# Kernel tuning notes

Hardware: AMD Instinct MI355X
Metric: run time of the kernel (lower is better)

## Reference

```python
import jax, jax.numpy as jnp
import numpy as np
jax.config.update("jax_enable_x64", True)

B, T, EPROJS, ODIM, U = 16, 1600, 512, 2048, 200
RISK_FACTOR = 0.1
NEG = float('-inf')


def _safe_lse0(x):
    # logsumexp over axis 0, safe for all -inf columns (no NaN in fwd or bwd)
    m = jnp.max(x, axis=0)
    ms = jnp.where(jnp.isinf(m), 0.0, m)
    s = jnp.sum(jnp.exp(x - ms), axis=0)
    out = ms + jnp.log(jnp.where(s == 0, 1.0, s))
    return jnp.where(s == 0, NEG, out)


def _log_sub_exp(a, b):
    # faithful port of log_substraction_exp: log(exp(a) - exp(b))
    mask1 = (~jnp.isinf(a)) & (~jnp.isinf(b))
    a_ = jnp.where(mask1, a, -1.0)
    b_ = jnp.where(mask1, b, -2.0)
    tmp = b_ + jnp.log(jnp.exp(a_ - b_) - 1.0)
    a_ = jnp.where(jnp.isinf(tmp), -2000.0, a_)
    b_ = jnp.where(jnp.isinf(tmp), -2001.0, b_)
    ans1 = b_ + jnp.log(jnp.exp(a_ - b_) - 1.0)
    ans = jnp.where(mask1, ans1, NEG)
    ans = jnp.where((~jnp.isinf(a)) & jnp.isinf(b), a, ans)
    return ans


def _ctc_bayes_loss(hs_pad, W, bvec, hlens, ys_pad):
    Bn, Tn, _ = hs_pad.shape
    Un = ys_pad.shape[1]
    S = 2 * Un + 1  # extended CTC state count (blank-interleaved)
    logits = hs_pad @ W.T + bvec
    logprob = jax.nn.log_softmax(logits, axis=-1).astype(jnp.float64)  # [B,T,V]
    ysc = jnp.where(ys_pad < 0, 0, ys_pad)
    olens = jnp.sum(ys_pad >= 0, axis=1)
    lp_blank = logprob[:, :, 0]                                        # [B,T]
    lp_label = jnp.take_along_axis(logprob, ysc[:, None, :], axis=2)   # [B,T,U]
    # emission log-probs on extended states: even=blank, odd=label u=(s-1)//2
    pair = jnp.stack([jnp.broadcast_to(lp_blank[:, :, None], (Bn, Tn, Un)), lp_label], axis=-1).reshape(Bn, Tn, 2 * Un)
    em = jnp.concatenate([pair, lp_blank[:, :, None]], axis=-1)        # [B,T,S]
    # skip transition (s-2 -> s) allowed into odd s with differing neighbor label
    allow_odd = jnp.concatenate([jnp.zeros((Bn, 1), bool), ysc[:, 1:] != ysc[:, :-1]], axis=1)
    allow = jnp.concatenate([jnp.stack([jnp.zeros((Bn, Un), bool), allow_odd], -1).reshape(Bn, 2 * Un), jnp.zeros((Bn, 1), bool)], axis=1)
    allow_fwd = jnp.concatenate([allow[:, 2:], jnp.zeros((Bn, 2), bool)], axis=1)
    em_t = jnp.transpose(em, (1, 0, 2))                                # [T,B,S]
    ninf2 = jnp.full((Bn, S), NEG, jnp.float64)
    alpha0 = ninf2.at[:, 0].set(em_t[0, :, 0]).at[:, 1].set(em_t[0, :, 1])

    def alpha_step(carry, e):
        s1 = jnp.concatenate([jnp.full((Bn, 1), NEG, jnp.float64), carry[:, :-1]], 1)
        s2 = jnp.concatenate([jnp.full((Bn, 2), NEG, jnp.float64), carry[:, :-2]], 1)
        s2 = jnp.where(allow, s2, NEG)
        new = e + _safe_lse0(jnp.stack([carry, s1, s2], 0))
        return new, new

    _, alpha_rest = jax.lax.scan(alpha_step, alpha0, em_t[1:])
    alpha_all = jnp.concatenate([alpha0[None], alpha_rest], 0)         # [T,B,S]

    sidx = jnp.arange(S)[None, :]
    fin = jnp.where((sidx == 2 * olens[:, None]) | (sidx == 2 * olens[:, None] - 1), 0.0, NEG)
    em_nxt = jnp.concatenate([em_t[1:], em_t[-1:]], 0)                 # em_nxt[t] = em_t[t+1]
    ts = jnp.arange(Tn - 1, -1, -1)

    def beta_step(carry, x):
        t, e_next = x
        g = e_next + carry
        g1 = jnp.concatenate([g[:, 1:], jnp.full((Bn, 1), NEG, jnp.float64)], 1)
        g2 = jnp.concatenate([g[:, 2:], jnp.full((Bn, 2), NEG, jnp.float64)], 1)
        g2 = jnp.where(allow_fwd, g2, NEG)
        new = _safe_lse0(jnp.stack([g, g1, g2], 0))
        new = jnp.where((t == hlens - 1)[:, None], fin, new)
        return new, new

    _, beta_rev = jax.lax.scan(beta_step, ninf2, (ts, em_nxt[::-1]))
    beta_all = beta_rev[::-1]                                          # [T,B,S]

    alpha_u = jnp.transpose(alpha_all, (1, 2, 0))[:, 1::2, :]          # [B,U,T]
    beta_u = jnp.transpose(beta_all, (1, 2, 0))[:, 1::2, :]
    valid = (jnp.arange(Un)[None, :, None] < olens[:, None, None]) & (jnp.arange(Tn)[None, None, :] < hlens[:, None, None])
    alpha_u = jnp.where(valid, alpha_u, NEG)
    beta_u = jnp.where(valid, beta_u, NEG)
    p = jnp.where(valid, jnp.transpose(lp_label, (0, 2, 1)), NEG)      # [B,U,T]
    beta_prime = jnp.concatenate([_log_sub_exp(beta_u[:, :, :-1], beta_u[:, :, 1:] + p[:, :, 1:]), beta_u[:, :, -1:]], axis=-1)
    risk = jnp.arange(1, Tn + 1, dtype=jnp.float64)[None, None, :] / hlens[:, None, None].astype(jnp.float64) * RISK_FACTOR
    loss_state = alpha_u + beta_prime + risk
    loss_state = jnp.where(jnp.isnan(loss_state), NEG, loss_state)
    # aggregate == 'time': logsumexp over t, pick last valid label position
    m = jnp.max(loss_state, axis=2)
    ms = jnp.where(jnp.isinf(m), 0.0, m)
    ssum = jnp.sum(jnp.exp(loss_state - ms[:, :, None]), axis=2)
    loss_u = jnp.where(ssum == 0, NEG, ms + jnp.log(jnp.where(ssum == 0, 1.0, ssum)))
    mask = jnp.isinf(loss_u)
    last = jnp.sum(~mask, axis=1) - 1
    loss_fsas = loss_u[jnp.arange(Bn), last]
    loss_fsas = jnp.where(hlens < olens, 0.0, loss_fsas)
    return jnp.mean(-loss_fsas)


def setup_inputs() -> dict:
    key = jax.random.key(0)
    k1, k2, k3, k4, k5, k6 = jax.random.split(key, 6)
    hs_pad = jax.random.normal(k1, (B, T, EPROJS), jnp.float32)
    W = jax.random.normal(k2, (ODIM, EPROJS), jnp.float32) * 0.05
    b = jnp.zeros((ODIM,), jnp.float32)
    hlens = (T - jax.random.randint(k3, (B,), 0, 200)).astype(jnp.int64)
    ys = jax.random.randint(k4, (B, U), 1, ODIM)
    olens = U - jax.random.randint(k5, (B,), 0, 20)
    ys_pad = jnp.where(jnp.arange(U)[None, :] < olens[:, None], ys, -1).astype(jnp.int64)
    ali = jax.random.randint(k6, (B, U), 0, T).astype(jnp.int64)
    return {"hs_pad": hs_pad, "W": W, "b": b, "hlens": hlens, "ys_pad": ys_pad, "ali": ali}


def reference(hs_pad, W, b, hlens, ys_pad, ali):
    # ali is unused for risk_strategy='time' (matches the torch module)
    return _ctc_bayes_loss(hs_pad, W, b, hlens, ys_pad)
```

## Files before the change

### kernel.cpp

```cpp
#include <hip/hip_runtime.h>
#include <math.h>


#define Bn    16
#define Tn    1600
#define NE    512
#define OD    2048
#define Un    200
#define Sn    401
#define NLAB  201
#define NGC   256

#define NEGINF (-INFINITY)
#define LSE_SUB_CONST_F (-2000.4586715f)

typedef short bf8_t  __attribute__((ext_vector_type(8)));
typedef float f32x4  __attribute__((ext_vector_type(4)));

__device__ __forceinline__ unsigned short f2bf(float x) {
    unsigned int u = __float_as_uint(x);
    unsigned int r = (u + 0x7FFFu + ((u >> 16) & 1u)) >> 16;
    return (unsigned short)r;
}
__device__ __forceinline__ void lse_merge_v(float& M, float& S, float v) {
    if (v > M) { S = S * __expf(M - v) + 1.f; M = v; }
    else       { S += __expf(v - M); }
}
__device__ __forceinline__ void lse_merge_ms(float& M, float& S, float m2, float s2) {
    if (s2 > 0.f) {
        if (m2 > M) { S = S * __expf(M - m2) + s2; M = m2; }
        else        { S += s2 * __expf(m2 - M); }
    }
}

__global__ __launch_bounds__(256)
void cast_hs_kernel(const float* __restrict__ src, unsigned short* __restrict__ dst, int n8) {
    int i = blockIdx.x * 256 + threadIdx.x;
    if (i >= n8) return;
    const float4* s4 = (const float4*)(src + (size_t)i * 8);
    float4 a = s4[0], b = s4[1];
    uint4 o;
    o.x = f2bf(a.x) | ((unsigned)f2bf(a.y) << 16);
    o.y = f2bf(a.z) | ((unsigned)f2bf(a.w) << 16);
    o.z = f2bf(b.x) | ((unsigned)f2bf(b.y) << 16);
    o.w = f2bf(b.z) | ((unsigned)f2bf(b.w) << 16);
    *(uint4*)(dst + (size_t)i * 8) = o;
}

__global__ __launch_bounds__(64)
void gather_kernel(const float* __restrict__ W, const float* __restrict__ bias,
                   const int* __restrict__ ys, unsigned short* __restrict__ Wgb,
                   float* __restrict__ biasg)
{
    const int b = blockIdx.x, j = blockIdx.y, tid = threadIdx.x;
    int col = -1;
    if (j == 0) col = 0;
    else if (j <= Un) { int y = ys[b * Un + j - 1]; col = (y < 0) ? 0 : y; }
    unsigned short* dst = Wgb + ((size_t)b * NGC + j) * NE;
    if (col >= 0) {
        const float* srcc = W + (size_t)col * NE;
        #pragma unroll
        for (int it = 0; it < 8; ++it) dst[tid + it * 64] = f2bf(srcc[tid + it * 64]);
    } else {
        #pragma unroll
        for (int it = 0; it < 8; ++it) dst[tid + it * 64] = 0;
    }
    if (tid == 0) biasg[b * NGC + j] = (col >= 0) ? bias[col] : 0.f;
}

#define KCH  64
#define ASTR 72

__global__ __launch_bounds__(256, 2)
void gemm_main_kernel(const unsigned short* __restrict__ hsb,
                      const unsigned short* __restrict__ Wb,
                      const float* __restrict__ bias,
                      float* __restrict__ Pm, float* __restrict__ Ps)
{
    __shared__ union {
        struct { unsigned short A[128 * ASTR]; unsigned short B[128 * ASTR]; } t;
        struct { float m[128 * 33]; float s[128 * 33]; } r;
    } sh;
    const int tid  = threadIdx.x;
    const int lane = tid & 63, w = tid >> 6;
    const int mw = w & 1, nw = w >> 1;
    const int quad = lane >> 4, lc = lane & 15;
    const int row0 = blockIdx.x * 128;
    const int c0   = blockIdx.y * 128;

    f32x4 acc[4][4];
    #pragma unroll
    for (int mi = 0; mi < 4; ++mi)
        #pragma unroll
        for (int ni = 0; ni < 4; ++ni) acc[mi][ni] = (f32x4)0.f;

    for (int kc = 0; kc < NE / KCH; ++kc) {
        __syncthreads();
        #pragma unroll
        for (int i = 0; i < 4; ++i) {
            int idx = tid + i * 256;
            int r = idx >> 3, c8 = idx & 7;
            *(uint4*)&sh.t.A[r * ASTR + c8 * 8] =
                *(const uint4*)&hsb[(size_t)(row0 + r) * NE + kc * KCH + c8 * 8];
            *(uint4*)&sh.t.B[r * ASTR + c8 * 8] =
                *(const uint4*)&Wb[(size_t)(c0 + r) * NE + kc * KCH + c8 * 8];
        }
        __syncthreads();
        #pragma unroll
        for (int ks = 0; ks < 2; ++ks) {
            bf8_t af[4], bg[4];
            #pragma unroll
            for (int mi = 0; mi < 4; ++mi)
                af[mi] = *(const bf8_t*)&sh.t.A[(mw * 64 + mi * 16 + lc) * ASTR + ks * 32 + quad * 8];
            #pragma unroll
            for (int ni = 0; ni < 4; ++ni)
                bg[ni] = *(const bf8_t*)&sh.t.B[(nw * 64 + ni * 16 + lc) * ASTR + ks * 32 + quad * 8];
            #pragma unroll
            for (int mi = 0; mi < 4; ++mi)
                #pragma unroll
                for (int ni = 0; ni < 4; ++ni)
                    acc[mi][ni] = __builtin_amdgcn_mfma_f32_16x16x32_bf16(af[mi], bg[ni], acc[mi][ni], 0, 0, 0);
        }
    }
    __syncthreads();
    float bcol[4];
    #pragma unroll
    for (int ni = 0; ni < 4; ++ni) bcol[ni] = bias[c0 + nw * 64 + ni * 16 + lc];
    #pragma unroll
    for (int mi = 0; mi < 4; ++mi)
        #pragma unroll
        for (int r = 0; r < 4; ++r) {
            float M = NEGINF, S = 0.f;
            #pragma unroll
            for (int ni = 0; ni < 4; ++ni) lse_merge_v(M, S, acc[mi][ni][r] + bcol[ni]);
            int rl = mw * 64 + mi * 16 + quad * 4 + r;
            sh.r.m[rl * 33 + nw * 16 + lc] = M;
            sh.r.s[rl * 33 + nw * 16 + lc] = S;
        }
    __syncthreads();
    if (tid < 128) {
        float M = NEGINF, S = 0.f;
        #pragma unroll 4
        for (int j = 0; j < 32; ++j) lse_merge_ms(M, S, sh.r.m[tid * 33 + j], sh.r.s[tid * 33 + j]);
        Pm[(size_t)blockIdx.y * 25600 + row0 + tid] = M;
        Ps[(size_t)blockIdx.y * 25600 + row0 + tid] = S;
    }
}

__global__ __launch_bounds__(256)
void lse_reduce_kernel(const float* __restrict__ Pm, const float* __restrict__ Ps,
                       float* __restrict__ lse)
{
    int row = blockIdx.x * 256 + threadIdx.x;
    float M = NEGINF, S = 0.f;
    #pragma unroll 4
    for (int nt = 0; nt < 16; ++nt)
        lse_merge_ms(M, S, Pm[(size_t)nt * 25600 + row], Ps[(size_t)nt * 25600 + row]);
    lse[row] = M + logf(S);
}

__global__ __launch_bounds__(256, 2)
void gemm_label_kernel(const unsigned short* __restrict__ hsb,
                       const unsigned short* __restrict__ Wgb,
                       const float* __restrict__ biasg, const float* __restrict__ lse,
                       float* __restrict__ lpl, float* __restrict__ lpbk)
{
    __shared__ unsigned short shA[64 * ASTR];
    __shared__ unsigned short shB[128 * ASTR];
    const int tid  = threadIdx.x;
    const int lane = tid & 63, w = tid >> 6;
    const int mw = w & 1, nw = w >> 1;
    const int quad = lane >> 4, lc = lane & 15;
    const int b  = blockIdx.x / 25, mt = blockIdx.x % 25;
    const int r0 = b * Tn + mt * 64;
    const int c0 = blockIdx.y * 128;

    f32x4 acc[2][4];
    #pragma unroll
    for (int mi = 0; mi < 2; ++mi)
        #pragma unroll
        for (int ni = 0; ni < 4; ++ni) acc[mi][ni] = (f32x4)0.f;

    const unsigned short* Wgbb = Wgb + (size_t)b * NGC * NE;
    for (int kc = 0; kc < NE / KCH; ++kc) {
        __syncthreads();
        #pragma unroll
        for (int i = 0; i < 2; ++i) {
            int idx = tid + i * 256;
            int r = idx >> 3, c8 = idx & 7;
            *(uint4*)&shA[r * ASTR + c8 * 8] =
                *(const uint4*)&hsb[(size_t)(r0 + r) * NE + kc * KCH + c8 * 8];
        }
        #pragma unroll
        for (int i = 0; i < 4; ++i) {
            int idx = tid + i * 256;
            int r = idx >> 3, c8 = idx & 7;
            *(uint4*)&shB[r * ASTR + c8 * 8] =
                *(const uint4*)&Wgbb[(size_t)(c0 + r) * NE + kc * KCH + c8 * 8];
        }
        __syncthreads();
        #pragma unroll
        for (int ks = 0; ks < 2; ++ks) {
            bf8_t af[2], bg[4];
            #pragma unroll
            for (int mi = 0; mi < 2; ++mi)
                af[mi] = *(const bf8_t*)&shA[(mw * 32 + mi * 16 + lc) * ASTR + ks * 32 + quad * 8];
            #pragma unroll
            for (int ni = 0; ni < 4; ++ni)
                bg[ni] = *(const bf8_t*)&shB[(nw * 64 + ni * 16 + lc) * ASTR + ks * 32 + quad * 8];
            #pragma unroll
            for (int mi = 0; mi < 2; ++mi)
                #pragma unroll
                for (int ni = 0; ni < 4; ++ni)
                    acc[mi][ni] = __builtin_amdgcn_mfma_f32_16x16x32_bf16(af[mi], bg[ni], acc[mi][ni], 0, 0, 0);
        }
    }
    #pragma unroll
    for (int mi = 0; mi < 2; ++mi)
        #pragma unroll
        for (int r = 0; r < 4; ++r) {
            int row = r0 + mw * 32 + mi * 16 + quad * 4 + r;
            float lsv = lse[row];
            #pragma unroll
            for (int ni = 0; ni < 4; ++ni) {
                int col = c0 + nw * 64 + ni * 16 + lc;
                if (col < NLAB) {
                    float v = acc[mi][ni][r] + biasg[b * NGC + col] - lsv;
                    if (col == 0) lpbk[row] = v;
                    else          lpl[(size_t)row * Un + (col - 1)] = v;
                }
            }
        }
}

#define IDX(s) ((s) + 2)

__device__ __forceinline__ float lse2f(float a, float b) {
    float mx = fmaxf(a, b);
    if (isinf(mx)) return NEGINF;
    return mx + __logf(__expf(a - mx) + __expf(b - mx));
}
__device__ __forceinline__ float lse3f(float v0, float v1, float v2) {
    float mx = fmaxf(v0, fmaxf(v1, v2));
    if (isinf(mx)) return NEGINF;
    return mx + __logf(__expf(v0 - mx) + __expf(v1 - mx) + __expf(v2 - mx));
}

#define STEP_BAR() do { \
    asm volatile("s_waitcnt lgkmcnt(0)" ::: "memory"); \
    __builtin_amdgcn_s_barrier(); \
    __builtin_amdgcn_sched_barrier(0); \
} while (0)

__global__ __launch_bounds__(256)
void scan_kernel(const float* __restrict__ lpl, const float* __restrict__ lpbk,
                 const int* __restrict__ hlens, const int* __restrict__ ys,
                 float* __restrict__ ast, float* __restrict__ bst)
{
    __shared__ float buf[2][408];
    __shared__ int   sh_olen, sh_hlen;

    const int b    = blockIdx.x & (Bn - 1);
    const int role = blockIdx.x >> 4;
    const int tid  = threadIdx.x;

    if (tid == 0) {
        int o = 0;
        for (int u = 0; u < Un; u++) if (ys[b * Un + u] >= 0) o++;
        sh_olen = o;
        sh_hlen = hlens[b];
    }
    for (int idx = tid; idx < 408; idx += 256) {
        buf[0][idx] = NEGINF;
        buf[1][idx] = NEGINF;
    }
    bool a1allow = false;
    if (tid >= 1 && tid < Un) {
        int y0 = ys[b * Un + tid - 1]; if (y0 < 0) y0 = 0;
        int y1 = ys[b * Un + tid];     if (y1 < 0) y1 = 0;
        a1allow = (y0 != y1);
    }
    bool a2allow = false;
    if (tid + 1 >= 1 && tid + 1 < Un) {
        int y0 = ys[b * Un + tid];     if (y0 < 0) y0 = 0;
        int y1 = ys[b * Un + tid + 1]; if (y1 < 0) y1 = 0;
        a2allow = (y0 != y1);
    }
    __syncthreads();

    const float* lplb = lpl + (size_t)b * Tn * Un;
    const float* lpbb = lpbk + (size_t)b * Tn;
    const int s0 = 2 * tid, s1 = 2 * tid + 1;
    const bool v0ok = (s0 < Sn);
    const bool v1ok = (s1 < Sn);
    const int  olen = sh_olen, hlen = sh_hlen;
    const int  ustar = olen - 1;

    if (role == 0) {
        float* as = ast + (size_t)b * Tn;
        if (tid == 0) { buf[0][IDX(0)] = lpbb[0]; buf[0][IDX(1)] = lplb[0]; }
        if (tid == ustar) as[0] = (tid == 0) ? lplb[0] : NEGINF;
        __syncthreads();

        #define ASTEP(T, EB, EO) do { \
            const float* cur = buf[((T) - 1) & 1]; \
            float* nxt = buf[(T) & 1]; \
            if (v0ok) { \
                float c1 = cur[IDX(s0) - 1]; \
                float c2 = cur[IDX(s0)], c3 = cur[IDX(s1)]; \
                float nv0 = lse2f(c2, c1); \
                if (!isinf(nv0)) nv0 += (EB); \
                nxt[IDX(s0)] = nv0; \
                if (v1ok) { \
                    float a1v2 = a1allow ? c1 : NEGINF; \
                    float nv1 = lse3f(c3, c2, a1v2); \
                    if (!isinf(nv1)) nv1 += (EO); \
                    nxt[IDX(s1)] = nv1; \
                    if (tid == ustar) as[T] = nv1; \
                } \
            } \
            STEP_BAR(); \
        } while (0)

        float ebA = lpbb[1], ebB = lpbb[2], ebC = lpbb[3], ebD = lpbb[4];
        float eoA = (tid < Un) ? lplb[(size_t)1 * Un + tid] : 0.f;
        float eoB = (tid < Un) ? lplb[(size_t)2 * Un + tid] : 0.f;
        float eoC = (tid < Un) ? lplb[(size_t)3 * Un + tid] : 0.f;
        float eoD = (tid < Un) ? lplb[(size_t)4 * Un + tid] : 0.f;
        int t = 1;
        for (; t + 3 < Tn; t += 4) {
            int rA = t + 4; if (rA > Tn - 1) rA = Tn - 1;
            float nbA = lpbb[rA];
            float noA = (tid < Un) ? lplb[(size_t)rA * Un + tid] : 0.f;
            ASTEP(t, ebA, eoA); ebA = nbA; eoA = noA;

            int rB = t + 5; if (rB > Tn - 1) rB = Tn - 1;
            float nbB = lpbb[rB];
            float noB = (tid < Un) ? lplb[(size_t)rB * Un + tid] : 0.f;
            ASTEP(t + 1, ebB, eoB); ebB = nbB; eoB = noB;

            int rC = t + 6; if (rC > Tn - 1) rC = Tn - 1;
            float nbC = lpbb[rC];
            float noC = (tid < Un) ? lplb[(size_t)rC * Un + tid] : 0.f;
            ASTEP(t + 2, ebC, eoC); ebC = nbC; eoC = noC;

            int rD = t + 7; if (rD > Tn - 1) rD = Tn - 1;
            float nbD = lpbb[rD];
            float noD = (tid < Un) ? lplb[(size_t)rD * Un + tid] : 0.f;
            ASTEP(t + 3, ebD, eoD); ebD = nbD; eoD = noD;
        }
        if (t < Tn)     ASTEP(t,     ebA, eoA);
        if (t + 1 < Tn) ASTEP(t + 1, ebB, eoB);
        if (t + 2 < Tn) ASTEP(t + 2, ebC, eoC);
        #undef ASTEP
    } else {
        float* bs = bst + (size_t)b * Tn;
        __syncthreads();

        #define BSTEP(T, EB, E0, E1) do { \
            const int it = (Tn - 1 - (T)) & 1; \
            const float* cur = buf[it]; \
            float* nxt = buf[it ^ 1]; \
            if (v0ok) { \
                float c0 = cur[IDX(s0)],     c1 = cur[IDX(s0) + 1]; \
                float c2 = cur[IDX(s0) + 2], c3 = cur[IDX(s0) + 3]; \
                float g0e = (EB) + c0; \
                float g1e = (E0) + c1; \
                float nv0 = lse2f(g0e, g1e); \
                float g0o = (E0) + c1; \
                float g1o = (EB) + c2; \
                float g2o = a2allow ? ((E1) + c3) : NEGINF; \
                float mh = fmaxf(g1o, g2o); \
                float h = NEGINF; \
                if (!isinf(mh)) \
                    h = mh + __logf(__expf(g1o - mh) + __expf(g2o - mh)); \
                float nv1 = v1ok ? lse3f(g0o, g1o, g2o) : NEGINF; \
                if ((T) == hlen - 1) { \
                    nv0 = (s0 == 2 * olen || s0 == 2 * olen - 1) ? 0.f : NEGINF; \
                    nv1 = (s1 == 2 * olen || s1 == 2 * olen - 1) ? 0.f : NEGINF; \
                } \
                nxt[IDX(s0)] = nv0; \
                if (v1ok) { \
                    nxt[IDX(s1)] = nv1; \
                    if (tid == ustar) { \
                        float bp; \
                        if ((T) >= hlen)          bp = NEGINF; \
                        else if ((T) == hlen - 1) bp = 0.f;  \
                        else if (isinf(g0o))      bp = h; \
                        else if (isinf(h))        bp = LSE_SUB_CONST_F; \
                        else { \
                            float sumlog = h - g0o; \
                            int k = (int)((__float_as_uint(fabsf(g0o)) >> 23) & 0xFF) - 127 - 53; \
                            if (k < -53) k = -53; \
                            bp = (sumlog > 709.7827f || sumlog < 0.69314718f * (float)k) \
                                 ? LSE_SUB_CONST_F : h; \
                        } \
                        bs[T] = bp; \
                    } \
                } \
            } \
            STEP_BAR(); \
        } while (0)

        float ebA = lpbb[Tn - 1];
        float e0A = (tid < Un)     ? lplb[(size_t)(Tn - 1) * Un + tid]     : 0.f;
        float e1A = (tid + 1 < Un) ? lplb[(size_t)(Tn - 1) * Un + tid + 1] : 0.f;
        float ebB = ebA, e0B = e0A, e1B = e1A;
        float ebC = lpbb[Tn - 2];
        float e0C = (tid < Un)     ? lplb[(size_t)(Tn - 2) * Un + tid]     : 0.f;
        float e1C = (tid + 1 < Un) ? lplb[(size_t)(Tn - 2) * Un + tid + 1] : 0.f;
        float ebD = lpbb[Tn - 3];
        float e0D = (tid < Un)     ? lplb[(size_t)(Tn - 3) * Un + tid]     : 0.f;
        float e1D = (tid + 1 < Un) ? lplb[(size_t)(Tn - 3) * Un + tid + 1] : 0.f;
        for (int t = Tn - 1; t > 0; t -= 4) {
            int rA = t - 3; if (rA < 0) rA = 0;
            float nbA = lpbb[rA];
            float n0A = (tid < Un)     ? lplb[(size_t)rA * Un + tid]     : 0.f;
            float n1A = (tid + 1 < Un) ? lplb[(size_t)rA * Un + tid + 1] : 0.f;
            BSTEP(t, ebA, e0A, e1A); ebA = nbA; e0A = n0A; e1A = n1A;

            int rB = t - 4; if (rB < 0) rB = 0;
            float nbB = lpbb[rB];
            float n0B = (tid < Un)     ? lplb[(size_t)rB * Un + tid]     : 0.f;
            float n1B = (tid + 1 < Un) ? lplb[(size_t)rB * Un + tid + 1] : 0.f;
            BSTEP(t - 1, ebB, e0B, e1B); ebB = nbB; e0B = n0B; e1B = n1B;

            int rC = t - 5; if (rC < 0) rC = 0;
            float nbC = lpbb[rC];
            float n0C = (tid < Un)     ? lplb[(size_t)rC * Un + tid]     : 0.f;
            float n1C = (tid + 1 < Un) ? lplb[(size_t)rC * Un + tid + 1] : 0.f;
            BSTEP(t - 2, ebC, e0C, e1C); ebC = nbC; e0C = n0C; e1C = n1C;

            int rD = t - 6; if (rD < 0) rD = 0;
            float nbD = lpbb[rD];
            float n0D = (tid < Un)     ? lplb[(size_t)rD * Un + tid]     : 0.f;
            float n1D = (tid + 1 < Un) ? lplb[(size_t)rD * Un + tid + 1] : 0.f;
            BSTEP(t - 3, ebD, e0D, e1D); ebD = nbD; e0D = n0D; e1D = n1D;
        }
        #undef BSTEP
    }
}

#define TCH 8
#define TPC (Tn / TCH)

__global__ __launch_bounds__(64)
void loss_kernel(const int* __restrict__ hlens, const int* __restrict__ ys,
                 const float* __restrict__ ast, const float* __restrict__ bst,
                 float* __restrict__ lossb)
{
    const int b = blockIdx.x, tid = threadIdx.x;
    __shared__ float sm[TCH], ss[TCH];
    __shared__ int sh_olen;
    if (tid == 0) {
        int o = 0;
        for (int u = 0; u < Un; u++) if (ys[b * Un + u] >= 0) o++;
        sh_olen = o;
    }
    __syncthreads();
    const int hlen = hlens[b];
    const float risk_c = 0.1f / (float)hlen;
    if (tid < TCH) {
        float m = NEGINF, s = 0.f;
        const float* as = ast + (size_t)b * Tn;
        const float* bs = bst + (size_t)b * Tn;
        const int t0 = tid * TPC, t1 = t0 + TPC;
        for (int t = t0; t < t1; ++t) {
            float v = as[t] + bs[t] + (float)(t + 1) * risk_c;
            if (!isinf(v)) lse_merge_v(m, s, v);
        }
        sm[tid] = m; ss[tid] = s;
    }
    __syncthreads();
    if (tid == 0) {
        float M = NEGINF, S = 0.f;
        #pragma unroll
        for (int c = 0; c < TCH; ++c) lse_merge_ms(M, S, sm[c], ss[c]);
        float lf = (S == 0.f) ? NEGINF : M + __logf(S);
        if (hlen < sh_olen) lf = 0.f;
        lossb[b] = lf;
    }
}

__global__ void finalize_kernel(const float* __restrict__ lossb, float* __restrict__ out) {
    if (threadIdx.x == 0 && blockIdx.x == 0) {
        float ssum = 0.f;
        for (int i = 0; i < Bn; i++) ssum += lossb[i];
        out[0] = -ssum / (float)Bn;
    }
}

extern "C" void kernel_launch(void* const* d_in, const int* in_sizes, int n_in,
                              void* d_out, int out_size, void* d_ws, size_t ws_size,
                              hipStream_t stream) {
    const float* hs    = (const float*)d_in[0];
    const float* W     = (const float*)d_in[1];
    const float* bias  = (const float*)d_in[2];
    const int*   hlens = (const int*)d_in[3];
    const int*   ys    = (const int*)d_in[4];
    float* out = (float*)d_out;

    char* p = (char*)d_ws;
    float* lpl    = (float*)p;  p += (size_t)25600 * Un * 4;
    float* lpbk   = (float*)p;  p += (size_t)25600 * 4;
    unsigned short* hsb = (unsigned short*)p; p += (size_t)25600 * NE * 2;
    unsigned short* Wb  = (unsigned short*)p; p += (size_t)OD * NE * 2;
    unsigned short* Wgb = (unsigned short*)p; p += (size_t)Bn * NGC * NE * 2;
    float* Pm    = (float*)p;   p += (size_t)16 * 25600 * 4;
    float* Ps    = (float*)p;   p += (size_t)16 * 25600 * 4;
    float* lse   = (float*)p;   p += (size_t)25600 * 4;
    float* biasg = (float*)p;   p += (size_t)Bn * NGC * 4;
    float* ast   = (float*)p;   p += (size_t)Bn * Tn * 4;
    float* bst   = (float*)p;   p += (size_t)Bn * Tn * 4;
    float* lossb = (float*)p;   p += 256;

    hipLaunchKernelGGL(cast_hs_kernel, dim3(6400), dim3(256), 0, stream,
                       hs, hsb, 25600 * NE / 8);
    hipLaunchKernelGGL(cast_hs_kernel, dim3(512), dim3(256), 0, stream,
                       W, Wb, OD * NE / 8);
    hipLaunchKernelGGL(gather_kernel, dim3(Bn, NGC), dim3(64), 0, stream,
                       W, bias, ys, Wgb, biasg);
    hipLaunchKernelGGL(gemm_main_kernel, dim3(200, 16), dim3(256), 0, stream,
                       hsb, Wb, bias, Pm, Ps);
    hipLaunchKernelGGL(lse_reduce_kernel, dim3(100), dim3(256), 0, stream,
                       Pm, Ps, lse);
    hipLaunchKernelGGL(gemm_label_kernel, dim3(400, 2), dim3(256), 0, stream,
                       hsb, Wgb, biasg, lse, lpl, lpbk);
    hipLaunchKernelGGL(scan_kernel, dim3(2 * Bn), dim3(256), 0, stream,
                       lpl, lpbk, hlens, ys, ast, bst);
    hipLaunchKernelGGL(loss_kernel, dim3(Bn), dim3(64), 0, stream,
                       hlens, ys, ast, bst, lossb);
    hipLaunchKernelGGL(finalize_kernel, dim3(1), dim3(64), 0, stream, lossb, out);
}
```

Baseline: 1.234 ms.

## Pad label logprobs to 256 stride, stage blank logprobs in LDS, shorten prefetch

Label log-probs are now stored with a padded row stride of 256, and the padding columns are zero-filled, so the scan kernels can load them without bounds checks. Blank log-probs for a batch are staged once into shared memory instead of being loaded from global memory every step. The scan's software prefetch depth drops from 4 to 2 steps, and the isinf guards before adding emissions are removed. This trims per-step instructions and global loads in the latency-bound serial scan, but prefetch latency hiding is shallower and the padded buffer is larger.

```diff
diff --git a/kernel.cpp b/kernel.cpp
--- a/kernel.cpp
+++ b/kernel.cpp
@@ -10,6 +10,7 @@
 #define Sn    401
 #define NLAB  201
 #define NGC   256
+#define LPS   256
 
 #define NEGINF (-INFINITY)
 #define LSE_SUB_CONST_F (-2000.4586715f)
@@ -224,11 +225,10 @@
             #pragma unroll
             for (int ni = 0; ni < 4; ++ni) {
                 int col = c0 + nw * 64 + ni * 16 + lc;
-                if (col < NLAB) {
-                    float v = acc[mi][ni][r] + biasg[b * NGC + col] - lsv;
-                    if (col == 0) lpbk[row] = v;
-                    else          lpl[(size_t)row * Un + (col - 1)] = v;
-                }
+                float v = acc[mi][ni][r] + biasg[b * NGC + col] - lsv;
+                if (col == 0)          lpbk[row] = v;
+                else if (col < NLAB)   lpl[(size_t)row * LPS + (col - 1)] = v;
+                else                   lpl[(size_t)row * LPS + (col - 1)] = 0.f;
             }
         }
 }
@@ -258,6 +258,7 @@
                  float* __restrict__ ast, float* __restrict__ bst)
 {
     __shared__ float buf[2][408];
+    __shared__ float ebs[Tn];
     __shared__ int   sh_olen, sh_hlen;
 
     const int b    = blockIdx.x & (Bn - 1);
@@ -274,6 +275,9 @@
         buf[0][idx] = NEGINF;
         buf[1][idx] = NEGINF;
     }
+    const float* lpbb = lpbk + (size_t)b * Tn;
+    for (int i = tid; i < Tn; i += 256) ebs[i] = lpbb[i];
+
     bool a1allow = false;
     if (tid >= 1 && tid < Un) {
         int y0 = ys[b * Un + tid - 1]; if (y0 < 0) y0 = 0;
@@ -288,8 +292,7 @@
     }
     __syncthreads();
 
-    const float* lplb = lpl + (size_t)b * Tn * Un;
-    const float* lpbb = lpbk + (size_t)b * Tn;
+    const float* lplb = lpl + (size_t)b * Tn * LPS;
     const int s0 = 2 * tid, s1 = 2 * tid + 1;
     const bool v0ok = (s0 < Sn);
     const bool v1ok = (s1 < Sn);
@@ -298,23 +301,21 @@
 
     if (role == 0) {
         float* as = ast + (size_t)b * Tn;
-        if (tid == 0) { buf[0][IDX(0)] = lpbb[0]; buf[0][IDX(1)] = lplb[0]; }
+        if (tid == 0) { buf[0][IDX(0)] = ebs[0]; buf[0][IDX(1)] = lplb[0]; }
         if (tid == ustar) as[0] = (tid == 0) ? lplb[0] : NEGINF;
         __syncthreads();
 
-        #define ASTEP(T, EB, EO) do { \
+        #define ASTEP(T, EO) do { \
             const float* cur = buf[((T) - 1) & 1]; \
             float* nxt = buf[(T) & 1]; \
             if (v0ok) { \
                 float c1 = cur[IDX(s0) - 1]; \
                 float c2 = cur[IDX(s0)], c3 = cur[IDX(s1)]; \
-                float nv0 = lse2f(c2, c1); \
-                if (!isinf(nv0)) nv0 += (EB); \
+                float nv0 = lse2f(c2, c1) + ebs[T]; \
                 nxt[IDX(s0)] = nv0; \
                 if (v1ok) { \
                     float a1v2 = a1allow ? c1 : NEGINF; \
-                    float nv1 = lse3f(c3, c2, a1v2); \
-                    if (!isinf(nv1)) nv1 += (EO); \
+                    float nv1 = lse3f(c3, c2, a1v2) + (EO); \
                     nxt[IDX(s1)] = nv1; \
                     if (tid == ustar) as[T] = nv1; \
                 } \
@@ -322,53 +323,35 @@
             STEP_BAR(); \
         } while (0)
 
-        float ebA = lpbb[1], ebB = lpbb[2], ebC = lpbb[3], ebD = lpbb[4];
-        float eoA = (tid < Un) ? lplb[(size_t)1 * Un + tid] : 0.f;
-        float eoB = (tid < Un) ? lplb[(size_t)2 * Un + tid] : 0.f;
-        float eoC = (tid < Un) ? lplb[(size_t)3 * Un + tid] : 0.f;
-        float eoD = (tid < Un) ? lplb[(size_t)4 * Un + tid] : 0.f;
-        int t = 1;
-        for (; t + 3 < Tn; t += 4) {
-            int rA = t + 4; if (rA > Tn - 1) rA = Tn - 1;
-            float nbA = lpbb[rA];
-            float noA = (tid < Un) ? lplb[(size_t)rA * Un + tid] : 0.f;
-            ASTEP(t, ebA, eoA); ebA = nbA; eoA = noA;
-
-            int rB = t + 5; if (rB > Tn - 1) rB = Tn - 1;
-            float nbB = lpbb[rB];
-            float noB = (tid < Un) ? lplb[(size_t)rB * Un + tid] : 0.f;
-            ASTEP(t + 1, ebB, eoB); ebB = nbB; eoB = noB;
-
-            int rC = t + 6; if (rC > Tn - 1) rC = Tn - 1;
-            float nbC = lpbb[rC];
-            float noC = (tid < Un) ? lplb[(size_t)rC * Un + tid] : 0.f;
-            ASTEP(t + 2, ebC, eoC); ebC = nbC; eoC = noC;
-
-            int rD = t + 7; if (rD > Tn - 1) rD = Tn - 1;
-            float nbD = lpbb[rD];
-            float noD = (tid < Un) ? lplb[(size_t)rD * Un + tid] : 0.f;
-            ASTEP(t + 3, ebD, eoD); ebD = nbD; eoD = noD;
-        }
-        if (t < Tn)     ASTEP(t,     ebA, eoA);
-        if (t + 1 < Tn) ASTEP(t + 1, ebB, eoB);
-        if (t + 2 < Tn) ASTEP(t + 2, ebC, eoC);
+        float eoA = lplb[(size_t)1 * LPS + tid];
+        float eoB = lplb[(size_t)2 * LPS + tid];
+        for (int t = 1; t < Tn; t += 2) {
+            int rA = t + 2; if (rA > Tn - 1) rA = Tn - 1;
+            float nA = lplb[(size_t)rA * LPS + tid];
+            ASTEP(t, eoA); eoA = nA;
+            if (t + 1 < Tn) {
+                int rB = t + 3; if (rB > Tn - 1) rB = Tn - 1;
+                float nB = lplb[(size_t)rB * LPS + tid];
+                ASTEP(t + 1, eoB); eoB = nB;
+            }
+        }
         #undef ASTEP
     } else {
         float* bs = bst + (size_t)b * Tn;
-        __syncthreads();
-
-        #define BSTEP(T, EB, E0, E1) do { \
+
+        #define BSTEP(T, E0, E1) do { \
             const int it = (Tn - 1 - (T)) & 1; \
             const float* cur = buf[it]; \
             float* nxt = buf[it ^ 1]; \
+            float eb = ebs[((T) + 1 > Tn - 1) ? (Tn - 1) : ((T) + 1)]; \
             if (v0ok) { \
                 float c0 = cur[IDX(s0)],     c1 = cur[IDX(s0) + 1]; \
                 float c2 = cur[IDX(s0) + 2], c3 = cur[IDX(s0) + 3]; \
-                float g0e = (EB) + c0; \
+                float g0e = eb + c0; \
                 float g1e = (E0) + c1; \
                 float nv0 = lse2f(g0e, g1e); \
                 float g0o = (E0) + c1; \
-                float g1o = (EB) + c2; \
+                float g1o = eb + c2; \
                 float g2o = a2allow ? ((E1) + c3) : NEGINF; \
                 float mh = fmaxf(g1o, g2o); \
                 float h = NEGINF; \
@@ -402,40 +385,21 @@
             STEP_BAR(); \
         } while (0)
 
-        float ebA = lpbb[Tn - 1];
-        float e0A = (tid < Un)     ? lplb[(size_t)(Tn - 1) * Un + tid]     : 0.f;
-        float e1A = (tid + 1 < Un) ? lplb[(size_t)(Tn - 1) * Un + tid + 1] : 0.f;
-        float ebB = ebA, e0B = e0A, e1B = e1A;
-        float ebC = lpbb[Tn - 2];
-        float e0C = (tid < Un)     ? lplb[(size_t)(Tn - 2) * Un + tid]     : 0.f;
-        float e1C = (tid + 1 < Un) ? lplb[(size_t)(Tn - 2) * Un + tid + 1] : 0.f;
-        float ebD = lpbb[Tn - 3];
-        float e0D = (tid < Un)     ? lplb[(size_t)(Tn - 3) * Un + tid]     : 0.f;
-        float e1D = (tid + 1 < Un) ? lplb[(size_t)(Tn - 3) * Un + tid + 1] : 0.f;
-        for (int t = Tn - 1; t > 0; t -= 4) {
-            int rA = t - 3; if (rA < 0) rA = 0;
-            float nbA = lpbb[rA];
-            float n0A = (tid < Un)     ? lplb[(size_t)rA * Un + tid]     : 0.f;
-            float n1A = (tid + 1 < Un) ? lplb[(size_t)rA * Un + tid + 1] : 0.f;
-            BSTEP(t, ebA, e0A, e1A); ebA = nbA; e0A = n0A; e1A = n1A;
-
-            int rB = t - 4; if (rB < 0) rB = 0;
-            float nbB = lpbb[rB];
-            float n0B = (tid < Un)     ? lplb[(size_t)rB * Un + tid]     : 0.f;
-            float n1B = (tid + 1 < Un) ? lplb[(size_t)rB * Un + tid + 1] : 0.f;
-            BSTEP(t - 1, ebB, e0B, e1B); ebB = nbB; e0B = n0B; e1B = n1B;
-
-            int rC = t - 5; if (rC < 0) rC = 0;
-            float nbC = lpbb[rC];
-            float n0C = (tid < Un)     ? lplb[(size_t)rC * Un + tid]     : 0.f;
-            float n1C = (tid + 1 < Un) ? lplb[(size_t)rC * Un + tid + 1] : 0.f;
-            BSTEP(t - 2, ebC, e0C, e1C); ebC = nbC; e0C = n0C; e1C = n1C;
-
-            int rD = t - 6; if (rD < 0) rD = 0;
-            float nbD = lpbb[rD];
-            float n0D = (tid < Un)     ? lplb[(size_t)rD * Un + tid]     : 0.f;
-            float n1D = (tid + 1 < Un) ? lplb[(size_t)rD * Un + tid + 1] : 0.f;
-            BSTEP(t - 3, ebD, e0D, e1D); ebD = nbD; e0D = n0D; e1D = n1D;
+        float e0A = lplb[(size_t)(Tn - 1) * LPS + tid];
+        float e1A = lplb[(size_t)(Tn - 1) * LPS + tid + 1];
+        float e0B = e0A, e1B = e1A;
+        for (int t = Tn - 1; t > 0; t -= 2) {
+            int rA = t - 1;
+            float n0A = lplb[(size_t)rA * LPS + tid];
+            float n1A = lplb[(size_t)rA * LPS + tid + 1];
+            BSTEP(t, e0A, e1A);
+            e0A = n0A; e1A = n1A;
+
+            int rB = t - 2; if (rB < 0) rB = 0;
+            float n0B = lplb[(size_t)rB * LPS + tid];
+            float n1B = lplb[(size_t)rB * LPS + tid + 1];
+            BSTEP(t - 1, e0B, e1B);
+            e0B = n0B; e1B = n1B;
         }
         #undef BSTEP
     }
@@ -501,7 +465,7 @@
     float* out = (float*)d_out;
 
     char* p = (char*)d_ws;
-    float* lpl    = (float*)p;  p += (size_t)25600 * Un * 4;
+    float* lpl    = (float*)p;  p += (size_t)25601 * LPS * 4;
     float* lpbk   = (float*)p;  p += (size_t)25600 * 4;
     unsigned short* hsb = (unsigned short*)p; p += (size_t)25600 * NE * 2;
     unsigned short* Wb  = (unsigned short*)p; p += (size_t)OD * NE * 2;
```

After: 1.202 ms. -2.6%, faster.
